# Kernel tuning notes

Hardware: AMD Instinct MI355X
Metric: run time of the kernel (lower is better)

The kernel has to match this reference:

```python
import jax, jax.numpy as jnp
import numpy as np

B, S, T = 32, 128, 64
H = 512
VS = VT = 32000


def _lstm_cell(x, h, c, W, U, b):
    # Keras LSTM gate order: i, f, g(cell), o
    z = x @ W + h @ U + b
    i, f, g, o = jnp.split(z, 4, axis=-1)
    c = jax.nn.sigmoid(f) * c + jax.nn.sigmoid(i) * jnp.tanh(g)
    h = jax.nn.sigmoid(o) * jnp.tanh(c)
    return h, c


def _lstm_scan(xs, h0, c0, W, U, b):
    # xs: [S, B, D]
    def step(carry, x):
        h, c = _lstm_cell(x, carry[0], carry[1], W, U, b)
        return (h, c), h
    (hT, cT), hs = jax.lax.scan(step, (h0, c0), xs)
    return hs, hT, cT


def setup_inputs() -> dict:
    key = jax.random.key(0)
    ks = jax.random.split(key, 16)
    def n(k, shape, s=0.02):
        return (jax.random.normal(k, shape, jnp.float32) * s).astype(jnp.float32)
    return {
        "src": jax.random.randint(ks[0], (B, S), 0, VS, jnp.int32),
        "trg": jax.random.randint(ks[1], (B, T), 0, VT, jnp.int32),
        "E_src": n(ks[2], (VS, H)),
        "E_trg": n(ks[3], (VT, H)),
        "Wf": n(ks[4], (H, 4 * H)), "Uf": n(ks[5], (H, 4 * H)), "bf": jnp.zeros((4 * H,), jnp.float32),
        "Wb": n(ks[6], (H, 4 * H)), "Ub": n(ks[7], (H, 4 * H)), "bb": jnp.zeros((4 * H,), jnp.float32),
        "Wd": n(ks[8], (H, 4 * H)), "Ud": n(ks[9], (H, 4 * H)), "bd": jnp.zeros((4 * H,), jnp.float32),
        "fcW": n(ks[10], (2 * H, H)), "fcb": jnp.zeros((H,), jnp.float32),
        "clsW": n(ks[11], (2 * H, VT)), "clsb": jnp.zeros((VT,), jnp.float32),
    }


def reference(src, trg, E_src, E_trg, Wf, Uf, bf, Wb, Ub, bb, Wd, Ud, bd, fcW, fcb, clsW, clsb):
    Bn = src.shape[0]
    Hn = E_src.shape[1]
    # --- Encoder: bidirectional LSTM ---
    xs = E_src[src].transpose(1, 0, 2)          # [S, B, H]
    z0 = jnp.zeros((Bn, Hn), xs.dtype)
    hs_f, hf, cf = _lstm_scan(xs, z0, z0, Wf, Uf, bf)
    hs_b, hb, cb = _lstm_scan(xs[::-1], z0, z0, Wb, Ub, bb)
    src_hidden = jnp.concatenate([hs_f, hs_b[::-1]], axis=-1).transpose(1, 0, 2)  # [B, S, 2H]
    # --- shared fc projections (same Dense, 2H -> H) ---
    src_h = src_hidden @ fcW + fcb                                   # [B, S, H]
    prev_h = jnp.concatenate([hf, hb], axis=-1) @ fcW + fcb          # [B, H]
    prev_c = jnp.concatenate([cf, cb], axis=-1) @ fcW + fcb          # [B, H]
    neg = jnp.where(src == 0, jnp.float32(-1e9), jnp.float32(0.0))   # [B, S]
    # --- Decoder (teacher forcing): per-step LSTM cell + dot-product attention ---
    ys = E_trg[trg[:, :-1]].transpose(1, 0, 2)  # [T-1, B, H]

    def step(carry, x):
        h, c = _lstm_cell(x, carry[0], carry[1], Wd, Ud, bd)
        score = jnp.einsum('bh,bsh->bs', h, src_h) + neg
        attn = jax.nn.softmax(score, axis=-1)
        ws = jnp.einsum('bs,bsh->bh', attn, src_h)
        return (h, c), jnp.concatenate([ws, h], axis=-1)  # dec_state [B, 2H]

    _, dec = jax.lax.scan(step, (prev_h, prev_c), ys)     # [T-1, B, 2H]
    logits = dec.transpose(1, 0, 2) @ clsW + clsb          # [B, T-1, VT]
    return logits
```

## Files before the change

### kernel.cpp

```cpp
#include <hip/hip_runtime.h>
#include <hip/hip_bf16.h>
#include <stdint.h>
#include <string.h>

constexpr int cB = 32, cS = 128, cT = 64, cH = 512, cH4 = 2048, cVT = 32000, cTM1 = 63;

typedef __attribute__((ext_vector_type(8))) __bf16 bf16x8;
typedef __attribute__((ext_vector_type(4))) float f32x4;

__device__ __forceinline__ float sigm(float x) { return 1.0f / (1.0f + expf(-x)); }

__device__ __forceinline__ bf16x8 sc_load16(const __hip_bfloat16* p) {
  bf16x8 r;
  asm volatile("global_load_dwordx4 %0, %1, off sc0 sc1"
               : "=&v"(r) : "v"(p) : "memory");
  return r;
}
__device__ __forceinline__ unsigned sc_load4u(const __hip_bfloat16* p) {
  unsigned r;
  asm volatile("global_load_dword %0, %1, off sc0 sc1"
               : "=&v"(r) : "v"(p) : "memory");
  return r;
}
__device__ __forceinline__ void sc_store4(__hip_bfloat16* p, unsigned v) {
  asm volatile("global_store_dword %0, %1, off sc0 sc1"
               :: "v"(p), "v"(v) : "memory");
}
__device__ __forceinline__ void pl_store4(__hip_bfloat16* p, unsigned v) {
  asm volatile("global_store_dword %0, %1, off"
               :: "v"(p), "v"(v) : "memory");
}
__device__ __forceinline__ unsigned sc_loadu(const unsigned* p) {
  unsigned r;
  asm volatile("global_load_dword %0, %1, off sc0 sc1"
               : "=&v"(r) : "v"(p) : "memory");
  asm volatile("s_waitcnt vmcnt(0)" ::: "memory");
  return r;
}
__device__ __forceinline__ void sc_storeu(unsigned* p, unsigned v) {
  asm volatile("global_store_dword %0, %1, off sc0 sc1"
               :: "v"(p), "v"(v) : "memory");
}

__device__ __forceinline__ void f2bT_tile(const float* __restrict__ src,
                                          __hip_bfloat16* __restrict__ dst,
                                          int K, int N, int gi, int bx, int by,
                                          float (*t)[33]) {
  int nt = bx * 32, kt = by * 32;
  int c = threadIdx.x & 31, r0 = threadIdx.x >> 5;
#pragma unroll
  for (int i = 0; i < 4; ++i) {
    int r = r0 + i * 8;
    t[r][c] = src[(size_t)(kt + r) * N + nt + c];
  }
  __syncthreads();
#pragma unroll
  for (int i = 0; i < 4; ++i) {
    int row = nt + r0 + i * 8;
    int pr = gi ? (((row & 511) << 2) | (row >> 9)) : row;
    dst[(size_t)pr * K + kt + c] = __float2bfloat16(t[c][r0 + i * 8]);
  }
  __syncthreads();
}

__device__ __forceinline__ void f2bT_tile512(const float* __restrict__ src,
                                             __hip_bfloat16* __restrict__ dst,
                                             int K, int N, int bx, int by,
                                             float (*t)[33]) {
  int nt = bx * 32, kt = by * 32;
  int c = threadIdx.x & 31, r0 = (threadIdx.x >> 5) & 15;
#pragma unroll
  for (int i = 0; i < 2; ++i) {
    int r = r0 + i * 16;
    t[r][c] = src[(size_t)(kt + r) * N + nt + c];
  }
  __syncthreads();
#pragma unroll
  for (int i = 0; i < 2; ++i) {
    int row = nt + r0 + i * 16;
    dst[(size_t)row * K + kt + c] = __float2bfloat16(t[c][r0 + i * 16]);
  }
  __syncthreads();
}

__global__ __launch_bounds__(256) void k_prep(
    const float* __restrict__ Wf, const float* __restrict__ Wb, const float* __restrict__ Wd,
    const float* __restrict__ Uf, const float* __restrict__ Ub, const float* __restrict__ Ud,
    const float* __restrict__ fcW,
    const float* __restrict__ bf, const float* __restrict__ bb, const float* __restrict__ bd,
    const int* __restrict__ src, const int* __restrict__ trg,
    const float* __restrict__ E_src, const float* __restrict__ E_trg,
    __hip_bfloat16* __restrict__ Wtfx, __hip_bfloat16* __restrict__ Wtbx,
    __hip_bfloat16* __restrict__ Wtdx,
    __hip_bfloat16* __restrict__ Utf, __hip_bfloat16* __restrict__ Utb,
    __hip_bfloat16* __restrict__ Utd,
    __hip_bfloat16* __restrict__ fcWt,
    float* __restrict__ bfx, float* __restrict__ bbx, float* __restrict__ bdx,
    __hip_bfloat16* __restrict__ xs_bf, __hip_bfloat16* __restrict__ ys_bf,
    float* __restrict__ neg, __hip_bfloat16* __restrict__ catb,
    unsigned* __restrict__ bars) {
  __shared__ float t[32][33];
  int id = blockIdx.x;
  int tid = threadIdx.x;
  if (id < 6144) {
    int grp = id >> 10, r = id & 1023;
    const float* s; __hip_bfloat16* d;
    switch (grp) {
      case 0: s = Wf; d = Wtfx; break;
      case 1: s = Wb; d = Wtbx; break;
      case 2: s = Wd; d = Wtdx; break;
      case 3: s = Uf; d = Utf; break;
      case 4: s = Ub; d = Utb; break;
      default: s = Ud; d = Utd; break;
    }
    f2bT_tile(s, d, 512, 2048, 1, r & 63, r >> 6, t);
  } else if (id < 6656) {
    int r = id - 6144;
    f2bT_tile(fcW, fcWt, 1024, 512, 0, r & 15, r >> 4, t);
  } else if (id < 6680) {
    int r = id - 6656;
    const float* s = (r < 8) ? bf : ((r < 16) ? bb : bd);
    float* d = (r < 8) ? bfx : ((r < 16) ? bbx : bdx);
    int i = (r & 7) * 256 + tid;
    d[i] = s[(i & 3) * 512 + (i >> 2)];
  } else if (id < 6744) {
    int r = id - 6680;
    ys_bf[(size_t)2016 * 512 + r * 256 + tid] = __float2bfloat16(0.0f);
  } else if (id < 6776) {
    int r = id - 6744;
    __hip_bfloat16* d = catb + (size_t)4160 * 1024 + (size_t)r * 2048 + tid * 8;
    bf16x8 zv = {};
    *(bf16x8*)d = zv;
  } else if (id < 8824) {
    int r = id - 6776;
    int half = tid >> 7, sb = 2 * r + half;
    int s = sb >> 5, b = sb & 31;
    int tok = src[b * cS + s];
    int cg = tid & 127;
    float4 e = ((const float4*)(E_src + (size_t)tok * cH))[cg];
    __hip_bfloat16* drow = xs_bf + (size_t)sb * cH + cg * 4;
    drow[0] = __float2bfloat16(e.x); drow[1] = __float2bfloat16(e.y);
    drow[2] = __float2bfloat16(e.z); drow[3] = __float2bfloat16(e.w);
    if (cg == 0) neg[b * cS + s] = (tok == 0) ? -1e9f : 0.0f;
  } else if (id < 9832) {
    int r = id - 8824;
    int half = tid >> 7, tb = 2 * r + half;
    int tt = tb >> 5, b = tb & 31;
    int tok = trg[b * cT + tt];
    int cg = tid & 127;
    float4 e = ((const float4*)(E_trg + (size_t)tok * cH))[cg];
    __hip_bfloat16* drow = ys_bf + (size_t)tb * cH + cg * 4;
    drow[0] = __float2bfloat16(e.x); drow[1] = __float2bfloat16(e.y);
    drow[2] = __float2bfloat16(e.z); drow[3] = __float2bfloat16(e.w);
  } else {
    if (tid < 64) bars[tid] = 0u;
  }
}

__global__ __launch_bounds__(256) void k_bgemm(const __hip_bfloat16* __restrict__ A,
                                               const __hip_bfloat16* __restrict__ Bt,
                                               const float* __restrict__ bias,
                                               float* __restrict__ C,
                                               int M, int K, int N) {
  __shared__ __hip_bfloat16 As[128 * 64];
  __shared__ __hip_bfloat16 Bs[128 * 64];
  const int tid = threadIdx.x;
  const int lane = tid & 63;
  const int wave = tid >> 6;
  const int wr = wave >> 1, wc = wave & 1;
  const int bm = blockIdx.x * 128, bn = blockIdx.y * 128;

  f32x4 acc[4][4] = {};

  const int srow = lane >> 3;
  const int scol = (lane & 7) * 8;

  for (int kt = 0; kt < K; kt += 64) {
#pragma unroll
    for (int i = 0; i < 4; ++i) {
      int c = wave * 4 + i;
      const __hip_bfloat16* ga = A + (size_t)(bm + c * 8 + srow) * K + kt + scol;
      __builtin_amdgcn_global_load_lds(
          (const __attribute__((address_space(1))) uint32_t*)ga,
          (__attribute__((address_space(3))) uint32_t*)(As + c * 512), 16, 0, 0);
      const __hip_bfloat16* gb = Bt + (size_t)(bn + c * 8 + srow) * K + kt + scol;
      __builtin_amdgcn_global_load_lds(
          (const __attribute__((address_space(1))) uint32_t*)gb,
          (__attribute__((address_space(3))) uint32_t*)(Bs + c * 512), 16, 0, 0);
    }
    __syncthreads();

#pragma unroll
    for (int kk = 0; kk < 64; kk += 32) {
      const int ko = kk + (lane >> 4) * 8;
      bf16x8 a[4], b[4];
      const int ar = wr * 64 + (lane & 15);
#pragma unroll
      for (int m = 0; m < 4; ++m)
        a[m] = *(const bf16x8*)(As + (size_t)(ar + m * 16) * 64 + ko);
      const int br = wc * 64 + (lane & 15);
#pragma unroll
      for (int n = 0; n < 4; ++n)
        b[n] = *(const bf16x8*)(Bs + (size_t)(br + n * 16) * 64 + ko);
#pragma unroll
      for (int m = 0; m < 4; ++m)
#pragma unroll
        for (int n = 0; n < 4; ++n)
          acc[m][n] = __builtin_amdgcn_mfma_f32_16x16x32_bf16(a[m], b[n], acc[m][n], 0, 0, 0);
    }
    __syncthreads();
  }

#pragma unroll
  for (int m = 0; m < 4; ++m) {
    const int row0 = bm + wr * 64 + m * 16 + (lane >> 4) * 4;
#pragma unroll
    for (int n = 0; n < 4; ++n) {
      const int col = bn + wc * 64 + n * 16 + (lane & 15);
      const float bv = bias[col];
#pragma unroll
      for (int r = 0; r < 4; ++r) {
        const int row = row0 + r;
        if (row < M) C[(size_t)row * N + col] = acc[m][n][r] + bv;
      }
    }
  }
}

__global__ __launch_bounds__(256) void k_bgemm2(
    const __hip_bfloat16* __restrict__ A,
    const __hip_bfloat16* __restrict__ Bt0, const __hip_bfloat16* __restrict__ Bt1,
    const float* __restrict__ bias0, const float* __restrict__ bias1,
    float* __restrict__ C0, float* __restrict__ C1,
    int M, int K, int N) {
  const __hip_bfloat16* Bt = blockIdx.z ? Bt1 : Bt0;
  const float* bias = blockIdx.z ? bias1 : bias0;
  float* C = blockIdx.z ? C1 : C0;

  __shared__ __hip_bfloat16 As[128 * 64];
  __shared__ __hip_bfloat16 Bs[128 * 64];
  const int tid = threadIdx.x;
  const int lane = tid & 63;
  const int wave = tid >> 6;
  const int wr = wave >> 1, wc = wave & 1;
  const int bm = blockIdx.x * 128, bn = blockIdx.y * 128;

  f32x4 acc[4][4] = {};
  const int srow = lane >> 3;
  const int scol = (lane & 7) * 8;

  for (int kt = 0; kt < K; kt += 64) {
#pragma unroll
    for (int i = 0; i < 4; ++i) {
      int c = wave * 4 + i;
      const __hip_bfloat16* ga = A + (size_t)(bm + c * 8 + srow) * K + kt + scol;
      __builtin_amdgcn_global_load_lds(
          (const __attribute__((address_space(1))) uint32_t*)ga,
          (__attribute__((address_space(3))) uint32_t*)(As + c * 512), 16, 0, 0);
      const __hip_bfloat16* gb = Bt + (size_t)(bn + c * 8 + srow) * K + kt + scol;
      __builtin_amdgcn_global_load_lds(
          (const __attribute__((address_space(1))) uint32_t*)gb,
          (__attribute__((address_space(3))) uint32_t*)(Bs + c * 512), 16, 0, 0);
    }
    __syncthreads();
#pragma unroll
    for (int kk = 0; kk < 64; kk += 32) {
      const int ko = kk + (lane >> 4) * 8;
      bf16x8 a[4], b[4];
      const int ar = wr * 64 + (lane & 15);
#pragma unroll
      for (int m = 0; m < 4; ++m)
        a[m] = *(const bf16x8*)(As + (size_t)(ar + m * 16) * 64 + ko);
      const int br = wc * 64 + (lane & 15);
#pragma unroll
      for (int n = 0; n < 4; ++n)
        b[n] = *(const bf16x8*)(Bs + (size_t)(br + n * 16) * 64 + ko);
#pragma unroll
      for (int m = 0; m < 4; ++m)
#pragma unroll
        for (int n = 0; n < 4; ++n)
          acc[m][n] = __builtin_amdgcn_mfma_f32_16x16x32_bf16(a[m], b[n], acc[m][n], 0, 0, 0);
    }
    __syncthreads();
  }
#pragma unroll
  for (int m = 0; m < 4; ++m) {
    const int row0 = bm + wr * 64 + m * 16 + (lane >> 4) * 4;
#pragma unroll
    for (int n = 0; n < 4; ++n) {
      const int col = bn + wc * 64 + n * 16 + (lane & 15);
      const float bv = bias[col];
#pragma unroll
      for (int r = 0; r < 4; ++r) {
        const int row = row0 + r;
        if (row < M) C[(size_t)row * N + col] = acc[m][n][r] + bv;
      }
    }
  }
}

#define SLOT_BARRIER(SLOTS, NB, GEN)                                             \
  {                                                                              \
    asm volatile("s_waitcnt vmcnt(2)" ::: "memory");                             \
    __builtin_amdgcn_sched_barrier(0);                                           \
    __builtin_amdgcn_s_barrier();                                                \
    if (tid == 0) sc_storeu((SLOTS) + (NB), (unsigned)(GEN));                    \
    if (wv == 0) {                                                               \
      for (;;) {                                                                 \
        unsigned v = sc_loadu((SLOTS) + (lane & 15));                            \
        if (__all((lane >= 16) | (v >= (unsigned)(GEN)))) break;                 \
        __builtin_amdgcn_s_sleep(1);                                             \
      }                                                                          \
    }                                                                            \
    __builtin_amdgcn_s_barrier();                                                \
    __builtin_amdgcn_sched_barrier(0);                                           \
  }

#define ENC_STEP(T, ZI0, ZI1, ZO0, ZO1)                                          \
  {                                                                              \
    const int t = (T);                                                           \
    const int trow = dir ? (127 - t) : t;                                        \
    if (t > 0) {                                                                 \
      const __hip_bfloat16* hsrc = hcur + (size_t)((t + 1) & 1) * 16384;         \
      bf16x8 hr[4];                                                              \
      _Pragma("unroll")                                                          \
      for (int i = 0; i < 4; ++i) {                                              \
        int c = tid + i * 512;                                                   \
        hr[i] = sc_load16(hsrc + (size_t)c * 8);                                 \
      }                                                                          \
      asm volatile("s_waitcnt vmcnt(0)" ::: "memory");                           \
      __builtin_amdgcn_sched_barrier(0);                                         \
      _Pragma("unroll")                                                          \
      for (int i = 0; i < 4; ++i) {                                              \
        int c = tid + i * 512;                                                   \
        int r = c >> 6, cc = (c & 63) * 8;                                       \
        *(bf16x8*)&Hs[r][cc] = hr[i];                                            \
      }                                                                          \
      asm volatile("s_waitcnt lgkmcnt(0)" ::: "memory");                         \
      __builtin_amdgcn_s_barrier();                                              \
      __builtin_amdgcn_sched_barrier(0);                                         \
    }                                                                            \
    f32x4 acc0 = {}, acc1 = {};                                                  \
    if (t > 0) {                                                                 \
      _Pragma("unroll")                                                          \
      for (int kk = 0; kk < 16; ++kk) {                                          \
        bf16x8 h0v = *(const bf16x8*)&Hs[b0][kk * 32 + fq * 8];                  \
        bf16x8 h1v = *(const bf16x8*)&Hs[b1][kk * 32 + fq * 8];                  \
        acc0 = __builtin_amdgcn_mfma_f32_16x16x32_bf16(afrag[kk], h0v, acc0, 0, 0, 0); \
        acc1 = __builtin_amdgcn_mfma_f32_16x16x32_bf16(afrag[kk], h1v, acc1, 0, 0, 0); \
      }                                                                          \
    }                                                                            \
    {                                                                            \
      float zi = ZI0[0] + acc0[0], zf = ZI0[1] + acc0[1],                        \
            zg = ZI0[2] + acc0[2], zo = ZI0[3] + acc0[3];                        \
      cs0 = sigm(zf) * cs0 + sigm(zi) * tanhf(zg);                               \
      Ho[b0][jloc] = __float2bfloat16(sigm(zo) * tanhf(cs0));                    \
    }                                                                            \
    {                                                                            \
      float zi = ZI1[0] + acc1[0], zf = ZI1[1] + acc1[1],                        \
            zg = ZI1[2] + acc1[2], zo = ZI1[3] + acc1[3];                        \
      cs1 = sigm(zf) * cs1 + sigm(zi) * tanhf(zg);                               \
      Ho[b1][jloc] = __float2bfloat16(sigm(zo) * tanhf(cs1));                    \
    }                                                                            \
    asm volatile("s_waitcnt lgkmcnt(0)" ::: "memory");                           \
    __builtin_amdgcn_s_barrier();                                                \
    __builtin_amdgcn_sched_barrier(0);                                           \
    {                                                                            \
      unsigned v = *(const unsigned*)&Ho[bb][jp];                                \
      sc_store4(hcur + (size_t)(t & 1) * 16384 + (size_t)bb * 512 + nb * 32 + jp, v); \
      pl_store4(catb + ((size_t)(bb * 128 + trow)) * 1024 + dhalf + nb * 32 + jp, v); \
    }                                                                            \
    __builtin_amdgcn_sched_barrier(0);                                           \
    const int tn = (t < 127) ? t + 1 : 127;                                      \
    const int ntrow = dir ? (127 - tn) : tn;                                     \
    ZO0 = *(const f32x4*)(xW + ((size_t)(ntrow * 32 + b0)) * 2048 + zc);         \
    ZO1 = *(const f32x4*)(xW + ((size_t)(ntrow * 32 + b1)) * 2048 + zc);         \
    if (t < 127) SLOT_BARRIER(slots, nb, t + 1);                                 \
  }

__global__ __launch_bounds__(512, 1) void k_enc_mfma(
    const float* __restrict__ xWf, const float* __restrict__ xWb,
    const __hip_bfloat16* __restrict__ Utf, const __hip_bfloat16* __restrict__ Utb,
    __hip_bfloat16* __restrict__ catb,
    __hip_bfloat16* __restrict__ henc,
    unsigned* bars,
    const __hip_bfloat16* __restrict__ ys_bf, const __hip_bfloat16* __restrict__ Wtdx,
    const float* __restrict__ bdx, float* __restrict__ yW) {
  __shared__ __hip_bfloat16 Hs[32][520];
  __shared__ __hip_bfloat16 Ho[32][36];
  __shared__ __hip_bfloat16 As[8192];
  __shared__ __hip_bfloat16 Bs[8192];

  const int tid = threadIdx.x;
  const int lane = tid & 63;
  const int wv = tid >> 6;

  if (blockIdx.x >= 32) {
    const int sidx = blockIdx.x - 32;
    const int wr = wv >> 2, wc = wv & 3;
    const int fr = lane & 15, fq = lane >> 4;
    for (int tile = sidx; tile < 256; tile += 224) {
      int bm = (tile & 15) * 128, bn = (tile >> 4) * 128;
      f32x4 acc[4][2] = {};
      for (int kt = 0; kt < 512; kt += 64) {
#pragma unroll
        for (int i = 0; i < 2; ++i) {
          int ch = wv * 2 + i;
          const __hip_bfloat16* ga = ys_bf + (size_t)(bm + ch * 8 + (lane >> 3)) * 512 + kt + (lane & 7) * 8;
          __builtin_amdgcn_global_load_lds(
              (const __attribute__((address_space(1))) uint32_t*)ga,
              (__attribute__((address_space(3))) uint32_t*)(As + ch * 512), 16, 0, 0);
          const __hip_bfloat16* gb = Wtdx + (size_t)(bn + ch * 8 + (lane >> 3)) * 512 + kt + (lane & 7) * 8;
          __builtin_amdgcn_global_load_lds(
              (const __attribute__((address_space(1))) uint32_t*)gb,
              (__attribute__((address_space(3))) uint32_t*)(Bs + ch * 512), 16, 0, 0);
        }
        __syncthreads();
#pragma unroll
        for (int kk = 0; kk < 64; kk += 32) {
          const int ko = kk + fq * 8;
          bf16x8 a[4], b[2];
#pragma unroll
          for (int m = 0; m < 4; ++m)
            a[m] = *(const bf16x8*)(As + (size_t)(wr * 64 + m * 16 + fr) * 64 + ko);
#pragma unroll
          for (int n = 0; n < 2; ++n)
            b[n] = *(const bf16x8*)(Bs + (size_t)(wc * 32 + n * 16 + fr) * 64 + ko);
#pragma unroll
          for (int m = 0; m < 4; ++m)
#pragma unroll
            for (int n = 0; n < 2; ++n)
              acc[m][n] = __builtin_amdgcn_mfma_f32_16x16x32_bf16(a[m], b[n], acc[m][n], 0, 0, 0);
        }
        __syncthreads();
      }
#pragma unroll
      for (int m = 0; m < 4; ++m) {
        const int row0 = bm + wr * 64 + m * 16 + fq * 4;
#pragma unroll
        for (int n = 0; n < 2; ++n) {
          const int col = bn + wc * 32 + n * 16 + fr;
          const float bv = bdx[col];
#pragma unroll
          for (int r = 0; r < 4; ++r)
            yW[(size_t)(row0 + r) * 2048 + col] = acc[m][n][r] + bv;
        }
      }
    }
    return;
  }

  const int bid = blockIdx.x;
  const int dir = bid >> 4, nb = bid & 15;
  const int c0 = nb * 128;
  const float* xW = dir ? xWb : xWf;
  const __hip_bfloat16* Ut = dir ? Utb : Utf;
  const int dhalf = dir * 512;
  __hip_bfloat16* hcur = henc + (size_t)dir * 32768;
  unsigned* slots = bars + dir * 16;

  const int fr = lane & 15;
  const int fq = lane >> 4;

  bf16x8 afrag[16];
#pragma unroll
  for (int kk = 0; kk < 16; ++kk)
    afrag[kk] = *(const bf16x8*)(Ut + (size_t)(c0 + wv * 16 + fr) * 512 + kk * 32 + fq * 8);

  const int jloc = wv * 4 + fq;
  const int b0 = fr, b1 = fr + 16;
  const int zc = c0 + wv * 16 + fq * 4;
  const int bb = tid >> 4, jp = (tid & 15) * 2;
  float cs0 = 0.f, cs1 = 0.f;

  const int trow0 = dir ? 127 : 0;
  f32x4 zA0 = *(const f32x4*)(xW + ((size_t)(trow0 * 32 + b0)) * 2048 + zc);
  f32x4 zA1 = *(const f32x4*)(xW + ((size_t)(trow0 * 32 + b1)) * 2048 + zc);
  f32x4 zB0, zB1;

  for (int it = 0; it < 64; ++it) {
    ENC_STEP(2 * it, zA0, zA1, zB0, zB1);
    ENC_STEP(2 * it + 1, zB0, zB1, zA0, zA1);
  }

  {
    unsigned v = *(const unsigned*)&Ho[bb][jp];
    pl_store4(catb + (size_t)(4096 + bb) * 1024 + dhalf + nb * 32 + jp, v);
  }
  __syncthreads();
  Ho[b0][jloc] = __float2bfloat16(cs0);
  Ho[b1][jloc] = __float2bfloat16(cs1);
  asm volatile("s_waitcnt lgkmcnt(0)" ::: "memory");
  __builtin_amdgcn_s_barrier();
  {
    unsigned v = *(const unsigned*)&Ho[bb][jp];
    pl_store4(catb + (size_t)(4128 + bb) * 1024 + dhalf + nb * 32 + jp, v);
  }
}

__device__ void attn_one(const float* __restrict__ src_h, const float* __restrict__ neg,
                         __hip_bfloat16* __restrict__ decb, int b, int t,
                         float* hv, float* sc, float* red) {
  const int tx = threadIdx.x;
  __hip_bfloat16* drow = decb + ((size_t)b * cTM1 + t) * 1024;
  if (tx < 256) {
    unsigned u = sc_load4u(drow + 512 + tx * 2);
    asm volatile("s_waitcnt vmcnt(0)" ::: "memory");
    hv[tx * 2] = __uint_as_float(u << 16);
    hv[tx * 2 + 1] = __uint_as_float(u & 0xffff0000u);
  }
  __syncthreads();
  {
    int s = tx >> 2, q = tx & 3;
    const float4* sr = (const float4*)(src_h + ((size_t)b * cS + s) * cH + q * 128);
    const float4* hh = (const float4*)(hv + q * 128);
    float acc = 0.f;
#pragma unroll 8
    for (int k = 0; k < 32; ++k) {
      float4 v = sr[k], h4 = hh[k];
      acc += v.x * h4.x + v.y * h4.y + v.z * h4.z + v.w * h4.w;
    }
    acc += __shfl_xor(acc, 1);
    acc += __shfl_xor(acc, 2);
    if (q == 0) {
      float s0 = acc + neg[b * cS + s];
      sc[s] = s0;
      red[s] = s0;
    }
  }
  __syncthreads();
  for (int off = 64; off >= 1; off >>= 1) {
    if (tx < off) red[tx] = fmaxf(red[tx], red[tx + off]);
    __syncthreads();
  }
  float mx = red[0];
  __syncthreads();
  float e = 0.f;
  if (tx < cS) { e = expf(sc[tx] - mx); red[tx] = e; }
  __syncthreads();
  for (int off = 64; off >= 1; off >>= 1) {
    if (tx < off) red[tx] += red[tx + off];
    __syncthreads();
  }
  float inv = 1.0f / red[0];
  __syncthreads();
  if (tx < cS) sc[tx] = e * inv;
  __syncthreads();
  {
    float a = 0.f;
    const float* sr = src_h + (size_t)b * cS * cH + tx;
    for (int s = 0; s < cS; ++s) a += sc[s] * sr[(size_t)s * cH];
    drow[tx] = __float2bfloat16(a);
  }
}

#define DEC_STEP(T, ZI0, ZI1, ZO0, ZO1)                                          \
  {                                                                              \
    const int t = (T);                                                           \
    if (t == 0) {                                                                \
      const float4* ph4 = (const float4*)prev_h;                                 \
      _Pragma("unroll")                                                          \
      for (int i = 0; i < 8; ++i) {                                              \
        int c = tid + i * 512;                                                   \
        float4 v = ph4[c];                                                       \
        int r = c >> 7, c4 = (c & 127) * 4;                                      \
        Hs[r][c4 + 0] = __float2bfloat16(v.x);                                   \
        Hs[r][c4 + 1] = __float2bfloat16(v.y);                                   \
        Hs[r][c4 + 2] = __float2bfloat16(v.z);                                   \
        Hs[r][c4 + 3] = __float2bfloat16(v.w);                                   \
      }                                                                          \
    } else {                                                                     \
      const __hip_bfloat16* hsrc = hdec + (size_t)((t + 1) & 1) * 16384;         \
      bf16x8 hr[4];                                                              \
      _Pragma("unroll")                                                          \
      for (int i = 0; i < 4; ++i) {                                              \
        int c = tid + i * 512;                                                   \
        hr[i] = sc_load16(hsrc + (size_t)c * 8);                                 \
      }                                                                          \
      asm volatile("s_waitcnt vmcnt(0)" ::: "memory");                           \
      __builtin_amdgcn_sched_barrier(0);                                         \
      _Pragma("unroll")                                                          \
      for (int i = 0; i < 4; ++i) {                                              \
        int c = tid + i * 512;                                                   \
        int r = c >> 6, cc = (c & 63) * 8;                                       \
        *(bf16x8*)&Hs[r][cc] = hr[i];                                            \
      }                                                                          \
    }                                                                            \
    asm volatile("s_waitcnt lgkmcnt(0)" ::: "memory");                           \
    __builtin_amdgcn_s_barrier();                                                \
    __builtin_amdgcn_sched_barrier(0);                                           \
    f32x4 acc0 = {}, acc1 = {};                                                  \
    _Pragma("unroll")                                                            \
    for (int kk = 0; kk < 16; ++kk) {                                            \
      bf16x8 h0v = *(const bf16x8*)&Hs[b0][kk * 32 + fq * 8];                    \
      bf16x8 h1v = *(const bf16x8*)&Hs[b1][kk * 32 + fq * 8];                    \
      acc0 = __builtin_amdgcn_mfma_f32_16x16x32_bf16(afrag[kk], h0v, acc0, 0, 0, 0); \
      acc1 = __builtin_amdgcn_mfma_f32_16x16x32_bf16(afrag[kk], h1v, acc1, 0, 0, 0); \
    }                                                                            \
    {                                                                            \
      float zi = ZI0[0] + acc0[0], zf = ZI0[1] + acc0[1],                        \
            zg = ZI0[2] + acc0[2], zo = ZI0[3] + acc0[3];                        \
      cs0 = sigm(zf) * cs0 + sigm(zi) * tanhf(zg);                               \
      Ho[b0][jloc] = __float2bfloat16(sigm(zo) * tanhf(cs0));                    \
    }                                                                            \
    {                                                                            \
      float zi = ZI1[0] + acc1[0], zf = ZI1[1] + acc1[1],                        \
            zg = ZI1[2] + acc1[2], zo = ZI1[3] + acc1[3];                        \
      cs1 = sigm(zf) * cs1 + sigm(zi) * tanhf(zg);                               \
      Ho[b1][jloc] = __float2bfloat16(sigm(zo) * tanhf(cs1));                    \
    }                                                                            \
    asm volatile("s_waitcnt lgkmcnt(0)" ::: "memory");                           \
    __builtin_amdgcn_s_barrier();                                                \
    __builtin_amdgcn_sched_barrier(0);                                           \
    {                                                                            \
      unsigned v = *(const unsigned*)&Ho[bb][jp];                                \
      sc_store4(hdec + (size_t)(t & 1) * 16384 + (size_t)bb * 512 + nb * 32 + jp, v); \
      sc_store4(decb + ((size_t)bb * cTM1 + t) * 1024 + 512 + nb * 32 + jp, v);  \
    }                                                                            \
    __builtin_amdgcn_sched_barrier(0);                                           \
    const int tn = (t < cTM1 - 1) ? t + 1 : cTM1 - 1;                            \
    ZO0 = *(const f32x4*)(yW + ((size_t)(tn * 32 + b0)) * 2048 + zc);            \
    ZO1 = *(const f32x4*)(yW + ((size_t)(tn * 32 + b1)) * 2048 + zc);            \
    if (t < cTM1 - 1) SLOT_BARRIER(slots, nb, t + 1);                            \
  }

__global__ __launch_bounds__(512, 1) void k_dec_mfma(
    const float* __restrict__ yW, const __hip_bfloat16* __restrict__ Utd,
    const float* __restrict__ prev_h, const float* __restrict__ prev_c,
    __hip_bfloat16* __restrict__ hdec, __hip_bfloat16* __restrict__ decb,
    const float* __restrict__ clsW, __hip_bfloat16* __restrict__ clsWt,
    const float* __restrict__ src_h, const float* __restrict__ neg,
    unsigned* slots) {
  __shared__ __hip_bfloat16 Hs[32][520];
  __shared__ __hip_bfloat16 Ho[32][36];
  __shared__ float tcv[32][33];
  __shared__ float hv_sh[512];
  __shared__ float sc_sh[128];
  __shared__ float red_sh[128];

  const int tid = threadIdx.x;
  const int lane = tid & 63;
  const int wv = tid >> 6;

  if (blockIdx.x >= 16) {
    const int sidx = blockIdx.x - 16;
    for (int tile = sidx; tile < 32000; tile += 240) {
      f2bT_tile512(clsW, clsWt, 1024, 32000, tile % 1000, tile / 1000, tcv);
    }
    unsigned waited = 0;
    for (int i = sidx; i < 2016; i += 240) {
      int t = i >> 5, b = i & 31;
      unsigned need = (unsigned)(t + 1);
      if (need > waited) {
        if (wv == 0) {
          for (;;) {
            unsigned v = sc_loadu(slots + (lane & 15));
            if (__all((lane >= 16) | (v >= need))) break;
            __builtin_amdgcn_s_sleep(4);
          }
        }
        __syncthreads();
        waited = need;
      }
      attn_one(src_h, neg, decb, b, t, hv_sh, sc_sh, red_sh);
    }
    return;
  }

  const int nb = blockIdx.x;
  const int c0 = nb * 128;
  const int fr = lane & 15;
  const int fq = lane >> 4;

  bf16x8 afrag[16];
#pragma unroll
  for (int kk = 0; kk < 16; ++kk)
    afrag[kk] = *(const bf16x8*)(Utd + (size_t)(c0 + wv * 16 + fr) * 512 + kk * 32 + fq * 8);

  const int jglob = nb * 32 + wv * 4 + fq;
  const int jloc = wv * 4 + fq;
  const int b0 = fr, b1 = fr + 16;
  const int zc = c0 + wv * 16 + fq * 4;
  const int bb = tid >> 4, jp = (tid & 15) * 2;
  float cs0 = prev_c[(size_t)b0 * 512 + jglob];
  float cs1 = prev_c[(size_t)b1 * 512 + jglob];

  f32x4 zA0 = *(const f32x4*)(yW + ((size_t)b0) * 2048 + zc);
  f32x4 zA1 = *(const f32x4*)(yW + ((size_t)b1) * 2048 + zc);
  f32x4 zB0, zB1;

  for (int it = 0; it < 31; ++it) {
    DEC_STEP(2 * it, zA0, zA1, zB0, zB1);
    DEC_STEP(2 * it + 1, zB0, zB1, zA0, zA1);
  }
  DEC_STEP(62, zA0, zA1, zB0, zB1);
  asm volatile("s_waitcnt vmcnt(0)" ::: "memory");
  __builtin_amdgcn_s_barrier();
  if (tid == 0) sc_storeu(slots + nb, (unsigned)cTM1);
}

extern "C" void kernel_launch(void* const* d_in, const int* in_sizes, int n_in,
                              void* d_out, int out_size, void* d_ws, size_t ws_size,
                              hipStream_t stream) {
  const int* src = (const int*)d_in[0];
  const int* trg = (const int*)d_in[1];
  const float* E_src = (const float*)d_in[2];
  const float* E_trg = (const float*)d_in[3];
  const float* Wf = (const float*)d_in[4];
  const float* Uf = (const float*)d_in[5];
  const float* bf = (const float*)d_in[6];
  const float* Wb = (const float*)d_in[7];
  const float* Ub = (const float*)d_in[8];
  const float* bb = (const float*)d_in[9];
  const float* Wd = (const float*)d_in[10];
  const float* Ud = (const float*)d_in[11];
  const float* bd = (const float*)d_in[12];
  const float* fcW = (const float*)d_in[13];
  const float* fcb = (const float*)d_in[14];
  const float* clsW = (const float*)d_in[15];
  const float* clsb = (const float*)d_in[16];
  float* out = (float*)d_out;
  float* ws = (float*)d_ws;

  float* xWf = ws;
  float* xWb = ws + 8388608;
  float* yW = ws + 16777216;
  float* neg = ws + 23035904;
  float* fco = ws + 23040000;
  __hip_bfloat16* decb = (__hip_bfloat16*)(ws + 25169920);
  __hip_bfloat16* Utd = (__hip_bfloat16*)(ws + 26218496);
  __hip_bfloat16* henc = (__hip_bfloat16*)(ws + 26742784);
  __hip_bfloat16* hdec = (__hip_bfloat16*)(ws + 26808320);
  unsigned* bars = (unsigned*)(ws + 26841088);
  float* pool = ws + 26841152;

  __hip_bfloat16* xs_bf = (__hip_bfloat16*)pool;
  __hip_bfloat16* ys_bf = (__hip_bfloat16*)(pool + 1048576);
  __hip_bfloat16* Utf = (__hip_bfloat16*)(pool + 1572864);
  __hip_bfloat16* Utb = (__hip_bfloat16*)(pool + 2097152);
  __hip_bfloat16* Wtfx = (__hip_bfloat16*)(pool + 2621440);
  __hip_bfloat16* Wtbx = (__hip_bfloat16*)(pool + 3145728);
  __hip_bfloat16* Wtdx = (__hip_bfloat16*)(pool + 3670016);
  float* bfx = pool + 4194304;
  float* bbx = pool + 4196352;
  float* bdx = pool + 4198400;
  __hip_bfloat16* fcWt = (__hip_bfloat16*)(pool + 4200448);
  __hip_bfloat16* cat_bf = (__hip_bfloat16*)(pool + 4462592);
  __hip_bfloat16* clsWt = (__hip_bfloat16*)xWf;

  k_prep<<<9833, 256, 0, stream>>>(Wf, Wb, Wd, Uf, Ub, Ud, fcW, bf, bb, bd,
                                   src, trg, E_src, E_trg,
                                   Wtfx, Wtbx, Wtdx, Utf, Utb, Utd, fcWt,
                                   bfx, bbx, bdx, xs_bf, ys_bf, neg, cat_bf, bars);

  k_bgemm2<<<dim3(32, 16, 2), 256, 0, stream>>>(xs_bf, Wtfx, Wtbx, bfx, bbx,
                                                xWf, xWb, 4096, 512, 2048);

  k_enc_mfma<<<256, 512, 0, stream>>>(xWf, xWb, Utf, Utb, cat_bf, henc, bars,
                                      ys_bf, Wtdx, bdx, yW);

  k_bgemm<<<dim3(33, 4), 256, 0, stream>>>(cat_bf, fcWt, fcb, fco, 4160, 1024, 512);

  const float* prev_h = fco + (size_t)4096 * 512;
  const float* prev_c = fco + (size_t)4128 * 512;
  k_dec_mfma<<<256, 512, 0, stream>>>(yW, Utd, prev_h, prev_c, hdec, decb,
                                      clsW, clsWt, fco, neg, bars + 32);

  k_bgemm<<<dim3(16, 250), 256, 0, stream>>>(decb, clsWt, clsb, out, 2016, 1024, 32000);
}
```

Before: 1.146 ms.

## Overlap decoder-h half of classifier GEMM with decoder recurrence in persistent kernel

Splits the final classifier GEMM along K. The h-half (decb columns 512-1023) is computed inside the decoder kernel by 144 idle blocks as soon as each group of 4 timesteps is ready, writing partial logits directly to the output. A separate kernel then adds the attention-context half plus bias with a read-modify-write. decb is reordered to time-major rows so each 128-row tile matches completed timesteps, and the clsW transpose moves to the new worker blocks. The cost is extra output traffic from the RMW pass and fewer blocks serving attention, which may lengthen the attention critical path.

```diff
diff --git a/kernel.cpp b/kernel.cpp
--- a/kernel.cpp
+++ b/kernel.cpp
@@ -227,6 +227,77 @@
   }
 }
 
+__global__ __launch_bounds__(256) void k_bgemm_ws(const __hip_bfloat16* __restrict__ A,
+                                                  const __hip_bfloat16* __restrict__ Bt,
+                                                  const float* __restrict__ bias,
+                                                  float* __restrict__ C) {
+  __shared__ __hip_bfloat16 As[128 * 64];
+  __shared__ __hip_bfloat16 Bs[128 * 64];
+  const int tid = threadIdx.x;
+  const int lane = tid & 63;
+  const int wave = tid >> 6;
+  const int wr = wave >> 1, wc = wave & 1;
+  const int bm = blockIdx.x * 128, bn = blockIdx.y * 128;
+
+  f32x4 acc[4][4] = {};
+  const int srow = lane >> 3;
+  const int scol = (lane & 7) * 8;
+
+  for (int kt = 0; kt < 512; kt += 64) {
+#pragma unroll
+    for (int i = 0; i < 4; ++i) {
+      int c = wave * 4 + i;
+      const __hip_bfloat16* ga = A + (size_t)(bm + c * 8 + srow) * 1024 + kt + scol;
+      __builtin_amdgcn_global_load_lds(
+          (const __attribute__((address_space(1))) uint32_t*)ga,
+          (__attribute__((address_space(3))) uint32_t*)(As + c * 512), 16, 0, 0);
+      const __hip_bfloat16* gb = Bt + (size_t)(bn + c * 8 + srow) * 1024 + kt + scol;
+      __builtin_amdgcn_global_load_lds(
+          (const __attribute__((address_space(1))) uint32_t*)gb,
+          (__attribute__((address_space(3))) uint32_t*)(Bs + c * 512), 16, 0, 0);
+    }
+    __syncthreads();
+#pragma unroll
+    for (int kk = 0; kk < 64; kk += 32) {
+      const int ko = kk + (lane >> 4) * 8;
+      bf16x8 a[4], b[4];
+      const int ar = wr * 64 + (lane & 15);
+#pragma unroll
+      for (int m = 0; m < 4; ++m)
+        a[m] = *(const bf16x8*)(As + (size_t)(ar + m * 16) * 64 + ko);
+      const int br = wc * 64 + (lane & 15);
+#pragma unroll
+      for (int n = 0; n < 4; ++n)
+        b[n] = *(const bf16x8*)(Bs + (size_t)(br + n * 16) * 64 + ko);
+#pragma unroll
+      for (int m = 0; m < 4; ++m)
+#pragma unroll
+        for (int n = 0; n < 4; ++n)
+          acc[m][n] = __builtin_amdgcn_mfma_f32_16x16x32_bf16(a[m], b[n], acc[m][n], 0, 0, 0);
+    }
+    __syncthreads();
+  }
+
+#pragma unroll
+  for (int m = 0; m < 4; ++m) {
+    const int row0 = bm + wr * 64 + m * 16 + (lane >> 4) * 4;
+#pragma unroll
+    for (int n = 0; n < 4; ++n) {
+      const int col = bn + wc * 64 + n * 16 + (lane & 15);
+      const float bv = bias[col];
+#pragma unroll
+      for (int r = 0; r < 4; ++r) {
+        const int row = row0 + r;
+        if (row < 2016) {
+          int orow = (row & 31) * 63 + (row >> 5);
+          float* cp = C + (size_t)orow * 32000 + col;
+          *cp = acc[m][n][r] + bv + *cp;
+        }
+      }
+    }
+  }
+}
+
 __global__ __launch_bounds__(256) void k_bgemm2(
     const __hip_bfloat16* __restrict__ A,
     const __hip_bfloat16* __restrict__ Bt0, const __hip_bfloat16* __restrict__ Bt1,
@@ -502,7 +573,7 @@
                          __hip_bfloat16* __restrict__ decb, int b, int t,
                          float* hv, float* sc, float* red) {
   const int tx = threadIdx.x;
-  __hip_bfloat16* drow = decb + ((size_t)b * cTM1 + t) * 1024;
+  __hip_bfloat16* drow = decb + ((size_t)(t * 32 + b)) * 1024;
   if (tx < 256) {
     unsigned u = sc_load4u(drow + 512 + tx * 2);
     asm volatile("s_waitcnt vmcnt(0)" ::: "memory");
@@ -615,7 +686,7 @@
     {                                                                            \
       unsigned v = *(const unsigned*)&Ho[bb][jp];                                \
       sc_store4(hdec + (size_t)(t & 1) * 16384 + (size_t)bb * 512 + nb * 32 + jp, v); \
-      sc_store4(decb + ((size_t)bb * cTM1 + t) * 1024 + 512 + nb * 32 + jp, v);  \
+      sc_store4(decb + ((size_t)(t * 32 + bb)) * 1024 + 512 + nb * 32 + jp, v);  \
     }                                                                            \
     __builtin_amdgcn_sched_barrier(0);                                           \
     const int tn = (t < cTM1 - 1) ? t + 1 : cTM1 - 1;                            \
@@ -630,6 +701,7 @@
     __hip_bfloat16* __restrict__ hdec, __hip_bfloat16* __restrict__ decb,
     const float* __restrict__ clsW, __hip_bfloat16* __restrict__ clsWt,
     const float* __restrict__ src_h, const float* __restrict__ neg,
+    float* __restrict__ outp,
     unsigned* slots) {
   __shared__ __hip_bfloat16 Hs[32][520];
   __shared__ __hip_bfloat16 Ho[32][36];
@@ -637,18 +709,112 @@
   __shared__ float hv_sh[512];
   __shared__ float sc_sh[128];
   __shared__ float red_sh[128];
+  __shared__ __hip_bfloat16 As[8192];
+  __shared__ __hip_bfloat16 Bs[8192];
 
   const int tid = threadIdx.x;
   const int lane = tid & 63;
   const int wv = tid >> 6;
 
+  if (blockIdx.x >= 112) {
+    const int k = blockIdx.x - 112;
+#pragma unroll 1
+    for (int pick = 0; pick < 2; ++pick) {
+      int bn = k + pick * 144;
+      if (bn >= 250) break;
+      for (int by = 0; by < 32; ++by)
+#pragma unroll 1
+        for (int sub = 0; sub < 4; ++sub)
+          f2bT_tile512(clsW, clsWt, 1024, 32000, bn * 4 + sub, by, tcv);
+    }
+    const int wr = wv >> 2, wc = wv & 3;
+    const int fr = lane & 15, fq = lane >> 4;
+#pragma unroll 1
+    for (int tm = 0; tm < 16; ++tm) {
+      unsigned need = (unsigned)(4 * tm + 4 > 63 ? 63 : 4 * tm + 4);
+      if (wv == 0) {
+        for (;;) {
+          unsigned v = sc_loadu(slots + (lane & 15));
+          if (__all((lane >= 16) | (v >= need))) break;
+          __builtin_amdgcn_s_sleep(4);
+        }
+      }
+      __syncthreads();
+#pragma unroll 1
+      for (int pick = 0; pick < 2; ++pick) {
+        int bn = k + pick * 144;
+        if (bn >= 250) break;
+        f32x4 acc[4][2] = {};
+        for (int kt = 0; kt < 512; kt += 64) {
+          bf16x8 ar[2];
+#pragma unroll
+          for (int i = 0; i < 2; ++i) {
+            int c = tid + i * 512;
+            int row = c >> 3, ko = (c & 7) * 8;
+            ar[i] = sc_load16(decb + (size_t)(tm * 128 + row) * 1024 + 512 + kt + ko);
+          }
+#pragma unroll
+          for (int i = 0; i < 2; ++i) {
+            int ch = wv * 2 + i;
+            const __hip_bfloat16* gb = clsWt + (size_t)(bn * 128 + ch * 8 + (lane >> 3)) * 1024 + 512 + kt + (lane & 7) * 8;
+            __builtin_amdgcn_global_load_lds(
+                (const __attribute__((address_space(1))) uint32_t*)gb,
+                (__attribute__((address_space(3))) uint32_t*)(Bs + ch * 512), 16, 0, 0);
+          }
+          asm volatile("s_waitcnt vmcnt(2)" ::: "memory");
+          __builtin_amdgcn_sched_barrier(0);
+#pragma unroll
+          for (int i = 0; i < 2; ++i) {
+            int c = tid + i * 512;
+            int row = c >> 3, ko = (c & 7) * 8;
+            *(bf16x8*)&As[row * 64 + ko] = ar[i];
+          }
+          asm volatile("s_waitcnt vmcnt(0) lgkmcnt(0)" ::: "memory");
+          __builtin_amdgcn_s_barrier();
+          __builtin_amdgcn_sched_barrier(0);
+#pragma unroll
+          for (int kk = 0; kk < 64; kk += 32) {
+            const int ko = kk + fq * 8;
+            bf16x8 a[4], b[2];
+#pragma unroll
+            for (int m = 0; m < 4; ++m)
+              a[m] = *(const bf16x8*)(As + (size_t)(wr * 64 + m * 16 + fr) * 64 + ko);
+#pragma unroll
+            for (int n = 0; n < 2; ++n)
+              b[n] = *(const bf16x8*)(Bs + (size_t)(wc * 32 + n * 16 + fr) * 64 + ko);
+#pragma unroll
+            for (int m = 0; m < 4; ++m)
+#pragma unroll
+              for (int n = 0; n < 2; ++n)
+                acc[m][n] = __builtin_amdgcn_mfma_f32_16x16x32_bf16(a[m], b[n], acc[m][n], 0, 0, 0);
+          }
+          __syncthreads();
+        }
+#pragma unroll
+        for (int m = 0; m < 4; ++m) {
+          const int row0 = tm * 128 + wr * 64 + m * 16 + fq * 4;
+#pragma unroll
+          for (int n = 0; n < 2; ++n) {
+            const int col = bn * 128 + wc * 32 + n * 16 + fr;
+#pragma unroll
+            for (int r = 0; r < 4; ++r) {
+              const int rrow = row0 + r;
+              if (rrow < 2016) {
+                int orow = (rrow & 31) * 63 + (rrow >> 5);
+                outp[(size_t)orow * 32000 + col] = acc[m][n][r];
+              }
+            }
+          }
+        }
+      }
+    }
+    return;
+  }
+
   if (blockIdx.x >= 16) {
     const int sidx = blockIdx.x - 16;
-    for (int tile = sidx; tile < 32000; tile += 240) {
-      f2bT_tile512(clsW, clsWt, 1024, 32000, tile % 1000, tile / 1000, tcv);
-    }
     unsigned waited = 0;
-    for (int i = sidx; i < 2016; i += 240) {
+    for (int i = sidx; i < 2016; i += 96) {
       int t = i >> 5, b = i & 31;
       unsigned need = (unsigned)(t + 1);
       if (need > waited) {
@@ -764,7 +930,7 @@
   const float* prev_h = fco + (size_t)4096 * 512;
   const float* prev_c = fco + (size_t)4128 * 512;
   k_dec_mfma<<<256, 512, 0, stream>>>(yW, Utd, prev_h, prev_c, hdec, decb,
-                                      clsW, clsWt, fco, neg, bars + 32);
-
-  k_bgemm<<<dim3(16, 250), 256, 0, stream>>>(decb, clsWt, clsb, out, 2016, 1024, 32000);
-}
+                                      clsW, clsWt, fco, neg, out, bars + 32);
+
+  k_bgemm_ws<<<dim3(16, 250), 256, 0, stream>>>(decb, clsWt, clsb, out);
+}
```

New measurement: 1.518 ms. 32.5% more time.
